# Performance work log

Hardware: AMD Instinct MI355X
Metric: run time of the kernel (lower is better)

Reference implementation:

```python
import jax, jax.numpy as jnp
import numpy as np

EMBED = 1024
HEADS = 16
HEAD_DIM = EMBED // HEADS
FFN_DIM = 4096
SEQ = 2048
BATCH = 2
EPS = 1e-5


def setup_inputs() -> dict:
    key = jax.random.key(0)
    ks = jax.random.split(key, 13)
    s = lambda n: 1.0 / np.sqrt(n)
    return {
        "x": jax.random.normal(ks[0], (BATCH, SEQ, EMBED), jnp.float32),
        # qkv projection (stored as [in, out])
        "w_qkv": jax.random.normal(ks[1], (EMBED, 3 * EMBED), jnp.float32) * s(EMBED),
        "b_qkv": jax.random.normal(ks[2], (3 * EMBED,), jnp.float32) * 0.02,
        "w_out": jax.random.normal(ks[3], (EMBED, EMBED), jnp.float32) * s(EMBED),
        "b_out": jax.random.normal(ks[4], (EMBED,), jnp.float32) * 0.02,
        # FFN
        "w_up": jax.random.normal(ks[5], (EMBED, FFN_DIM), jnp.float32) * s(EMBED),
        "b_up": jax.random.normal(ks[6], (FFN_DIM,), jnp.float32) * 0.02,
        "w_down": jax.random.normal(ks[7], (FFN_DIM, EMBED), jnp.float32) * s(FFN_DIM),
        "b_down": jax.random.normal(ks[8], (EMBED,), jnp.float32) * 0.02,
        # LayerNorms
        "g1": jnp.ones((EMBED,), jnp.float32),
        "be1": jnp.zeros((EMBED,), jnp.float32),
        "g2": jnp.ones((EMBED,), jnp.float32),
        "be2": jnp.zeros((EMBED,), jnp.float32),
    }


def _layernorm(x, g, b):
    mu = jnp.mean(x, axis=-1, keepdims=True)
    var = jnp.mean(jnp.square(x - mu), axis=-1, keepdims=True)
    return (x - mu) * jax.lax.rsqrt(var + EPS) * g + b


def reference(x, w_qkv, b_qkv, w_out, b_out, w_up, b_up, w_down, b_down, g1, be1, g2, be2):
    B, S, E = x.shape
    qkv = (x @ w_qkv + b_qkv).reshape(B, S, 3, HEADS, HEAD_DIM)
    qkv = jnp.transpose(qkv, (2, 0, 3, 1, 4))
    q, k, v = qkv[0], qkv[1], qkv[2]
    scale = 1.0 / jnp.sqrt(jnp.float32(HEAD_DIM))
    attn = jnp.einsum("bhqd,bhkd->bhqk", q, k) * scale  # [B,H,S,S]
    causal = jnp.tril(jnp.ones((S, S), bool))
    attn = jnp.where(causal, attn, -jnp.inf)
    attn = jax.nn.softmax(attn, axis=-1)
    out = jnp.einsum("bhqk,bhkd->bhqd", attn, v)  # [B,H,S,D]
    out = jnp.transpose(out, (0, 2, 1, 3)).reshape(B, S, E)
    attn_out = out @ w_out + b_out
    x = _layernorm(x + attn_out, g1, be1)
    ffn_out = jax.nn.relu(x @ w_up + b_up) @ w_down + b_down
    return _layernorm(x + ffn_out, g2, be2)
```

## Files before the change

### kernel.cpp

```cpp
#include <hip/hip_runtime.h>
#include <hip/hip_bf16.h>

#define EMBED 1024
#define HEADS 16
#define HDIM 64
#define FFN 4096
#define SEQ 2048
#define BATCH 2
#define MTOT (BATCH*SEQ)
#define QSCALE 0.1803368801111137f

typedef __attribute__((ext_vector_type(8))) short bf16x8;
typedef __attribute__((ext_vector_type(4))) float f32x4;
typedef __attribute__((ext_vector_type(16))) float f32x16;
typedef unsigned short u16;
typedef unsigned int u32;

__device__ __forceinline__ u16 f2bf(float f) {
  union { float f; unsigned u; } v; v.f = f;
  unsigned r = v.u + 0x7FFFu + ((v.u >> 16) & 1u);
  return (u16)(r >> 16);
}

__device__ __forceinline__ void async_ld16(const void* g, void* l) {
  __builtin_amdgcn_global_load_lds((const __attribute__((address_space(1))) void*)g,
                                   (__attribute__((address_space(3))) void*)l,
                                   16, 0, 0);
}

__global__ __launch_bounds__(256) void k_cvt(const float* __restrict__ in,
                                             u16* __restrict__ out, int n4) {
  int i = blockIdx.x * 256 + threadIdx.x;
  int st = gridDim.x * 256;
  for (; i < n4; i += st) {
    float4 v = ((const float4*)in)[i];
    ushort4 o;
    o.x = f2bf(v.x); o.y = f2bf(v.y); o.z = f2bf(v.z); o.w = f2bf(v.w);
    ((ushort4*)out)[i] = o;
  }
}

__global__ __launch_bounds__(256) void k_tr(const float* __restrict__ w,
                                            u16* __restrict__ wT, int K, int N) {
  __shared__ u16 tile[32][33];
  int n0 = blockIdx.x * 32, k0 = blockIdx.y * 32;
  int tx = threadIdx.x, ty = threadIdx.y;
  #pragma unroll
  for (int i = 0; i < 4; ++i) {
    int k = k0 + ty + i * 8;
    tile[ty + i * 8][tx] = f2bf(w[(size_t)k * N + n0 + tx]);
  }
  __syncthreads();
  #pragma unroll
  for (int i = 0; i < 4; ++i) {
    int n = n0 + ty + i * 8;
    wT[(size_t)n * K + k0 + tx] = tile[tx][ty + i * 8];
  }
}

__global__ __launch_bounds__(256) void k_vtr(const u16* __restrict__ V,
                                             u16* __restrict__ Vt) {
  __shared__ u16 t[64][72];
  const int s0 = blockIdx.x * 64;
  const size_t ib = (size_t)blockIdx.y * (size_t)SEQ * HDIM;
  const size_t ob = (size_t)blockIdx.y * (size_t)HDIM * SEQ;
  const int tid = threadIdx.x;
  const int r = tid >> 2, c0 = (tid & 3) * 16;
  bf16x8 v0 = *(const bf16x8*)(V + ib + (size_t)(s0 + r) * HDIM + c0);
  bf16x8 v1 = *(const bf16x8*)(V + ib + (size_t)(s0 + r) * HDIM + c0 + 8);
  #pragma unroll
  for (int j = 0; j < 8; ++j) {
    t[c0 + j][r] = (u16)v0[j];
    t[c0 + 8 + j][r] = (u16)v1[j];
  }
  __syncthreads();
  const int d = tid >> 2, sc = (tid & 3) * 16;
  bf16x8 o0, o1;
  #pragma unroll
  for (int j = 0; j < 8; ++j) { o0[j] = t[d][sc + j]; o1[j] = t[d][sc + 8 + j]; }
  *(bf16x8*)(Vt + ob + (size_t)d * SEQ + s0 + sc) = o0;
  *(bf16x8*)(Vt + ob + (size_t)d * SEQ + s0 + sc + 8) = o1;
}

template <int BN, int BK, int OMODE, bool RELU>
__global__ __launch_bounds__(256) void k_gemm(
    const u16* __restrict__ A, const u16* __restrict__ BT,
    const float* __restrict__ bias,
    void* __restrict__ out0, void* __restrict__ out1, void* __restrict__ out2,
    int M, int N, int K) {
  constexpr int NR = BN / 32;
  constexpr int KS = BK / 32;
  constexpr int TPR = BK / 8;
  constexpr int RPI = 256 / TPR;
  constexpr int CM = TPR - 1;

  __shared__ u16 As[2][128 * BK];
  __shared__ u16 Bs[2][BN * BK];
  const int tid = threadIdx.x;
  const int lane = tid & 63, g = lane >> 4, li = lane & 15;
  const int wid = tid >> 6, wm = wid >> 1, wn = wid & 1;

  const int gx = gridDim.x;
  const int nwg = gx * gridDim.y;
  const int flat = blockIdx.y * gx + blockIdx.x;
  const int cpx = nwg >> 3;
  const int swz = (flat & 7) * cpx + (flat >> 3);
  const int m0 = (swz / gx) * 128, n0 = (swz % gx) * BN;

  f32x4 acc[4][NR] = {};

  const u16* Ablk = A + (size_t)m0 * K;
  const u16* Bblk = BT + (size_t)n0 * K;
  const int srow = tid / TPR;
  const int scol = ((tid % TPR) ^ (srow & CM)) * 8;

  auto stage = [&](int buf, int kt) {
    #pragma unroll
    for (int r = 0; r < 128; r += RPI)
      async_ld16(Ablk + (size_t)(srow + r) * K + kt + scol, &As[buf][(srow + r) * BK] + (tid % TPR) * 8);
    #pragma unroll
    for (int r = 0; r < BN; r += RPI)
      async_ld16(Bblk + (size_t)(srow + r) * K + kt + scol, &Bs[buf][(srow + r) * BK] + (tid % TPR) * 8);
  };

  stage(0, 0);
  int cur = 0;
  for (int kt = 0; kt < K; kt += BK) {
    __syncthreads();
    if (kt + BK < K) stage(cur ^ 1, kt + BK);

    bf16x8 af[4][KS], bfr[NR][KS];
    #pragma unroll
    for (int i = 0; i < 4; ++i) {
      const int row = wm * 64 + i * 16 + li;
      #pragma unroll
      for (int ks = 0; ks < KS; ++ks) {
        const int c = ks * 4 + g;
        af[i][ks] = *(const bf16x8*)(&As[cur][row * BK] + ((c ^ (row & CM)) & CM) * 8);
      }
    }
    #pragma unroll
    for (int j = 0; j < NR; ++j) {
      const int row = wn * (BN / 2) + j * 16 + li;
      #pragma unroll
      for (int ks = 0; ks < KS; ++ks) {
        const int c = ks * 4 + g;
        bfr[j][ks] = *(const bf16x8*)(&Bs[cur][row * BK] + ((c ^ (row & CM)) & CM) * 8);
      }
    }
    #pragma unroll
    for (int ks = 0; ks < KS; ++ks)
      #pragma unroll
      for (int i = 0; i < 4; ++i)
        #pragma unroll
        for (int j = 0; j < NR; ++j)
          acc[i][j] = __builtin_amdgcn_mfma_f32_16x16x32_bf16(af[i][ks], bfr[j][ks], acc[i][j], 0, 0, 0);
    cur ^= 1;
  }

  float bcol[NR];
  #pragma unroll
  for (int j = 0; j < NR; ++j) bcol[j] = bias[n0 + wn * (BN / 2) + j * 16 + li];

  #pragma unroll
  for (int i = 0; i < 4; ++i) {
    #pragma unroll
    for (int j = 0; j < NR; ++j) {
      #pragma unroll
      for (int r = 0; r < 4; ++r) {
        int row = m0 + wm * 64 + i * 16 + g * 4 + r;
        int col = n0 + wn * (BN / 2) + j * 16 + li;
        float v = acc[i][j][r] + bcol[j];
        if (RELU) v = fmaxf(v, 0.f);
        if (OMODE == 0) {
          ((u16*)out0)[(size_t)row * N + col] = f2bf(v);
        } else if (OMODE == 1) {
          ((float*)out0)[(size_t)row * N + col] = v;
        } else {
          int which = col >> 10, hh = (col >> 6) & 15, d = col & 63;
          int bb = row >> 11, ss = row & 2047;
          if (which == 0) v *= QSCALE;
          u16* dst = which == 0 ? (u16*)out0 : (which == 1 ? (u16*)out1 : (u16*)out2);
          dst[((size_t)((bb * 16 + hh) * 2048 + ss)) * 64 + d] = f2bf(v);
        }
      }
    }
  }
}

__global__ __launch_bounds__(256, 3) void k_attn6(
    const u16* __restrict__ Q, const u16* __restrict__ K,
    const u16* __restrict__ Vt, u16* __restrict__ ctx) {
  const int bh = blockIdx.x;
  const int t32 = 63 - (int)blockIdx.y;
  const int b = bh >> 4, h = bh & 15;
  const int tid = threadIdx.x;
  const int wid = tid >> 6, lane = tid & 63;
  const int ql = lane & 31, hl = lane >> 5;

  __shared__ __align__(16) float mrg[3][64][34];

  const int wq0 = t32 * 32;
  const int qg = wq0 + ql;
  const int nt = ((wq0 + 31) >> 6) + 1;

  const size_t kbase = (size_t)bh * SEQ * HDIM;
  const size_t vbase = (size_t)bh * HDIM * SEQ;

  bf16x8 qf[4];
  #pragma unroll
  for (int d4 = 0; d4 < 4; ++d4)
    qf[d4] = *(const bf16x8*)(Q + kbase + (size_t)qg * HDIM + d4 * 16 + hl * 8);

  const u16* kp = K + kbase + (size_t)ql * HDIM + hl * 8;
  const u16* vp = Vt + vbase + (size_t)ql * SEQ + hl * 8;

  f32x16 o0 = {}, o1 = {};
  float m_run = -1e30f, l_run = 0.f;

  for (int kt = wid; kt < nt; kt += 4) {
    const bool kh1 = (kt * 64 + 32 <= wq0 + 31);
    const bool domask = (kt * 64 + (kh1 ? 63 : 31) > wq0);
    const int koff = kt * 64 * HDIM;

    bf16x8 kf0[4], kf1[4];
    #pragma unroll
    for (int d4 = 0; d4 < 4; ++d4) {
      kf0[d4] = *(const bf16x8*)(kp + koff + d4 * 16);
      if (kh1) kf1[d4] = *(const bf16x8*)(kp + koff + 32 * HDIM + d4 * 16);
    }
    bf16x8 vf0[4], vf1[4];
    #pragma unroll
    for (int t = 0; t < 4; ++t)
      if (t < 2 || kh1) {
        vf0[t] = *(const bf16x8*)(vp + kt * 64 + t * 16);
        vf1[t] = *(const bf16x8*)(vp + 32 * SEQ + kt * 64 + t * 16);
      }

    f32x16 S0 = {}, S1 = {};
    #pragma unroll
    for (int d4 = 0; d4 < 4; ++d4)
      S0 = __builtin_amdgcn_mfma_f32_32x32x16_bf16(kf0[d4], qf[d4], S0, 0, 0, 0);
    if (kh1) {
      #pragma unroll
      for (int d4 = 0; d4 < 4; ++d4)
        S1 = __builtin_amdgcn_mfma_f32_32x32x16_bf16(kf1[d4], qf[d4], S1, 0, 0, 0);
    }

    if (domask) {
      const int qrel = qg - kt * 64 - 4 * hl;
      #pragma unroll
      for (int r = 0; r < 16; ++r) {
        const int kc = (r & 3) + 8 * (r >> 2);
        S0[r] = (kc <= qrel) ? S0[r] : -3.0e38f;
      }
      if (kh1) {
        #pragma unroll
        for (int r = 0; r < 16; ++r) {
          const int kc = 32 + (r & 3) + 8 * (r >> 2);
          S1[r] = (kc <= qrel) ? S1[r] : -3.0e38f;
        }
      }
    }

    float mt = -3.0e38f;
    #pragma unroll
    for (int r = 0; r < 16; ++r) mt = fmaxf(mt, S0[r]);
    if (kh1) {
      #pragma unroll
      for (int r = 0; r < 16; ++r) mt = fmaxf(mt, S1[r]);
    }
    mt = fmaxf(mt, __shfl_xor(mt, 32, 64));

    if (!__all(mt <= m_run + 8.0f)) {
      const float mn = fmaxf(m_run, mt);
      const float alpha = exp2f(m_run - mn);
      l_run *= alpha;
      o0 *= alpha;
      o1 *= alpha;
      m_run = mn;
    }
    float sum = 0.f;
    #pragma unroll
    for (int r = 0; r < 16; ++r) { S0[r] = exp2f(S0[r] - m_run); sum += S0[r]; }
    if (kh1) {
      #pragma unroll
      for (int r = 0; r < 16; ++r) { S1[r] = exp2f(S1[r] - m_run); sum += S1[r]; }
    }
    sum += __shfl_xor(sum, 32, 64);
    l_run += sum;

    u32 pk[2][8], sw[2][8];
    #pragma unroll
    for (int m = 0; m < 4; ++m) {
      asm("v_cvt_pk_bf16_f32 %0, %1, %2" : "=v"(pk[0][2*m])   : "v"(S0[4*m+0]), "v"(S0[4*m+1]));
      asm("v_cvt_pk_bf16_f32 %0, %1, %2" : "=v"(pk[0][2*m+1]) : "v"(S0[4*m+2]), "v"(S0[4*m+3]));
    }
    #pragma unroll
    for (int i = 0; i < 8; ++i) sw[0][i] = __shfl_xor(pk[0][i], 32, 64);
    if (kh1) {
      #pragma unroll
      for (int m = 0; m < 4; ++m) {
        asm("v_cvt_pk_bf16_f32 %0, %1, %2" : "=v"(pk[1][2*m])   : "v"(S1[4*m+0]), "v"(S1[4*m+1]));
        asm("v_cvt_pk_bf16_f32 %0, %1, %2" : "=v"(pk[1][2*m+1]) : "v"(S1[4*m+2]), "v"(S1[4*m+3]));
      }
      #pragma unroll
      for (int i = 0; i < 8; ++i) sw[1][i] = __shfl_xor(pk[1][i], 32, 64);
    }

    #pragma unroll
    for (int t = 0; t < 4; ++t) {
      if (t < 2 || kh1) {
        const int c = t >> 1, m0 = 2 * (t & 1), m1 = m0 + 1;
        union { u32 u[4]; bf16x8 v; } pf;
        pf.u[0] = hl ? sw[c][2*m1]   : pk[c][2*m0];
        pf.u[1] = hl ? sw[c][2*m1+1] : pk[c][2*m0+1];
        pf.u[2] = hl ? pk[c][2*m1]   : sw[c][2*m0];
        pf.u[3] = hl ? pk[c][2*m1+1] : sw[c][2*m0+1];
        o0 = __builtin_amdgcn_mfma_f32_32x32x16_bf16(vf0[t], pf.v, o0, 0, 0, 0);
        o1 = __builtin_amdgcn_mfma_f32_32x32x16_bf16(vf1[t], pf.v, o1, 0, 0, 0);
      }
    }
  }

  if (wid > 0) {
    float* p = &mrg[wid - 1][lane][0];
    *(f32x16*)(p) = o0;
    *(f32x16*)(p + 16) = o1;
    p[32] = m_run;
    p[33] = l_run;
  }
  __syncthreads();
  if (wid > 0) return;

  float M = m_run;
  #pragma unroll
  for (int w = 0; w < 3; ++w) M = fmaxf(M, mrg[w][lane][32]);
  const float fa = exp2f(m_run - M);
  f32x16 acc0 = o0 * fa, acc1 = o1 * fa;
  float L = l_run * fa;
  #pragma unroll
  for (int w = 0; w < 3; ++w) {
    const float* p = &mrg[w][lane][0];
    const float fw = exp2f(p[32] - M);
    L += p[33] * fw;
    f32x16 t0 = *(const f32x16*)(p);
    f32x16 t1 = *(const f32x16*)(p + 16);
    acc0 += t0 * fw;
    acc1 += t1 * fw;
  }
  const float inv = 1.f / L;

  u16* outp = ctx + (size_t)(b * SEQ + qg) * EMBED + h * HDIM + 4 * hl;
  #pragma unroll
  for (int m = 0; m < 4; ++m) {
    ushort4 s0v, s1v;
    s0v.x = f2bf(acc0[4*m+0] * inv); s0v.y = f2bf(acc0[4*m+1] * inv);
    s0v.z = f2bf(acc0[4*m+2] * inv); s0v.w = f2bf(acc0[4*m+3] * inv);
    *(ushort4*)(outp + 8 * m) = s0v;
    s1v.x = f2bf(acc1[4*m+0] * inv); s1v.y = f2bf(acc1[4*m+1] * inv);
    s1v.z = f2bf(acc1[4*m+2] * inv); s1v.w = f2bf(acc1[4*m+3] * inv);
    *(ushort4*)(outp + 32 + 8 * m) = s1v;
  }
}

__global__ __launch_bounds__(256) void k_add_ln(
    const float* __restrict__ a, const float* __restrict__ bmat,
    const float* __restrict__ gam, const float* __restrict__ bet,
    float* __restrict__ outf, u16* __restrict__ outb) {
  const int row = blockIdx.x;
  const int t = threadIdx.x;
  __shared__ float red[8];
  float4 va = ((const float4*)(a + (size_t)row * EMBED))[t];
  float4 vb = ((const float4*)(bmat + (size_t)row * EMBED))[t];
  float s0 = va.x + vb.x, s1 = va.y + vb.y, s2 = va.z + vb.z, s3 = va.w + vb.w;
  float sum = s0 + s1 + s2 + s3;
  float sq = s0 * s0 + s1 * s1 + s2 * s2 + s3 * s3;
  #pragma unroll
  for (int m = 1; m < 64; m <<= 1) {
    sum += __shfl_xor(sum, m, 64);
    sq += __shfl_xor(sq, m, 64);
  }
  int wid = t >> 6;
  if ((t & 63) == 0) { red[wid] = sum; red[4 + wid] = sq; }
  __syncthreads();
  sum = red[0] + red[1] + red[2] + red[3];
  sq = red[4] + red[5] + red[6] + red[7];
  float mean = sum * (1.f / EMBED);
  float var = sq * (1.f / EMBED) - mean * mean;
  float rstd = rsqrtf(var + 1e-5f);
  float4 gv = ((const float4*)gam)[t], bev = ((const float4*)bet)[t];
  float y0 = (s0 - mean) * rstd * gv.x + bev.x;
  float y1 = (s1 - mean) * rstd * gv.y + bev.y;
  float y2 = (s2 - mean) * rstd * gv.z + bev.z;
  float y3 = (s3 - mean) * rstd * gv.w + bev.w;
  float4 o; o.x = y0; o.y = y1; o.z = y2; o.w = y3;
  ((float4*)(outf + (size_t)row * EMBED))[t] = o;
  if (outb) {
    ushort4 ob; ob.x = f2bf(y0); ob.y = f2bf(y1); ob.z = f2bf(y2); ob.w = f2bf(y3);
    ((ushort4*)(outb + (size_t)row * EMBED))[t] = ob;
  }
}

extern "C" void kernel_launch(void* const* d_in, const int* in_sizes, int n_in,
                              void* d_out, int out_size, void* d_ws, size_t ws_size,
                              hipStream_t stream) {
  const float* x      = (const float*)d_in[0];
  const float* w_qkv  = (const float*)d_in[1];
  const float* b_qkv  = (const float*)d_in[2];
  const float* w_out  = (const float*)d_in[3];
  const float* b_out  = (const float*)d_in[4];
  const float* w_up   = (const float*)d_in[5];
  const float* b_up   = (const float*)d_in[6];
  const float* w_down = (const float*)d_in[7];
  const float* b_down = (const float*)d_in[8];
  const float* g1  = (const float*)d_in[9];
  const float* be1 = (const float*)d_in[10];
  const float* g2  = (const float*)d_in[11];
  const float* be2 = (const float*)d_in[12];

  char* ws = (char*)d_ws;
  size_t off = 0;
  auto alloc = [&](size_t bytes) { void* p = ws + off; off += (bytes + 255) & ~(size_t)255; return p; };

  u16* xb     = (u16*)alloc((size_t)MTOT * EMBED * 2);
  u16* wqkvT  = (u16*)alloc((size_t)3 * EMBED * EMBED * 2);
  u16* woutT  = (u16*)alloc((size_t)EMBED * EMBED * 2);
  u16* wupT   = (u16*)alloc((size_t)FFN * EMBED * 2);
  u16* wdownT = (u16*)alloc((size_t)EMBED * FFN * 2);
  u16* qb     = (u16*)alloc((size_t)MTOT * EMBED * 2);
  u16* kb     = (u16*)alloc((size_t)MTOT * EMBED * 2);
  u16* vb     = (u16*)alloc((size_t)MTOT * EMBED * 2);
  u16* vtb    = (u16*)alloc((size_t)MTOT * EMBED * 2);
  u16* ctx    = (u16*)alloc((size_t)MTOT * EMBED * 2);
  float* attn_proj = (float*)alloc((size_t)MTOT * EMBED * 4);
  float* y_f32     = (float*)alloc((size_t)MTOT * EMBED * 4);
  u16* y_bf16      = (u16*)alloc((size_t)MTOT * EMBED * 2);
  u16* hmid        = (u16*)alloc((size_t)MTOT * FFN * 2);
  float* ffn_o     = (float*)alloc((size_t)MTOT * EMBED * 4);

  dim3 trb(32, 8);
  k_cvt<<<2048, 256, 0, stream>>>(x, xb, MTOT * EMBED / 4);
  k_tr<<<dim3(3 * EMBED / 32, EMBED / 32), trb, 0, stream>>>(w_qkv, wqkvT, EMBED, 3 * EMBED);
  k_tr<<<dim3(EMBED / 32, EMBED / 32), trb, 0, stream>>>(w_out, woutT, EMBED, EMBED);
  k_tr<<<dim3(FFN / 32, EMBED / 32), trb, 0, stream>>>(w_up, wupT, EMBED, FFN);
  k_tr<<<dim3(EMBED / 32, FFN / 32), trb, 0, stream>>>(w_down, wdownT, FFN, EMBED);

  k_gemm<128, 32, 2, false><<<dim3(3 * EMBED / 128, MTOT / 128), 256, 0, stream>>>(
      xb, wqkvT, b_qkv, qb, kb, vb, MTOT, 3 * EMBED, EMBED);

  k_vtr<<<dim3(SEQ / 64, BATCH * HEADS), 256, 0, stream>>>(vb, vtb);

  k_attn6<<<dim3(BATCH * HEADS, 64), 256, 0, stream>>>(qb, kb, vtb, ctx);

  k_gemm<64, 64, 1, false><<<dim3(EMBED / 64, MTOT / 128), 256, 0, stream>>>(
      ctx, woutT, b_out, attn_proj, nullptr, nullptr, MTOT, EMBED, EMBED);

  k_add_ln<<<MTOT, 256, 0, stream>>>(x, attn_proj, g1, be1, y_f32, y_bf16);

  k_gemm<128, 32, 0, true><<<dim3(FFN / 128, MTOT / 128), 256, 0, stream>>>(
      y_bf16, wupT, b_up, hmid, nullptr, nullptr, MTOT, FFN, EMBED);

  k_gemm<64, 64, 1, false><<<dim3(EMBED / 64, MTOT / 128), 256, 0, stream>>>(
      hmid, wdownT, b_down, ffn_o, nullptr, nullptr, MTOT, EMBED, FFN);

  k_add_ln<<<MTOT, 256, 0, stream>>>(y_f32, ffn_o, g2, be2, (float*)d_out, nullptr);

  (void)in_sizes; (void)n_in; (void)out_size; (void)ws_size;
}
```

Baseline: 277.8 us.

## Add 256x256-tile 8-wave GEMM with ping-pong staging for QKV and FFN-up

```diff
diff --git a/kernel.cpp b/kernel.cpp
--- a/kernel.cpp
+++ b/kernel.cpp
@@ -80,6 +80,141 @@
   for (int j = 0; j < 8; ++j) { o0[j] = t[d][sc + j]; o1[j] = t[d][sc + 8 + j]; }
   *(bf16x8*)(Vt + ob + (size_t)d * SEQ + s0 + sc) = o0;
   *(bf16x8*)(Vt + ob + (size_t)d * SEQ + s0 + sc + 8) = o1;
+}
+
+template <int OMODE, bool RELU>
+__global__ __launch_bounds__(512) void k_gemm8(
+    const u16* __restrict__ A, const u16* __restrict__ BT,
+    const float* __restrict__ bias,
+    void* __restrict__ out0, void* __restrict__ out1, void* __restrict__ out2,
+    int M, int N, int K) {
+  __shared__ __align__(16) u16 As[2][2][128 * 64];
+  __shared__ __align__(16) u16 Bs[2][2][128 * 64];
+  const int tid = threadIdx.x;
+  const int lane = tid & 63, g = lane >> 4, li = lane & 15;
+  const int wid = tid >> 6, wm = wid >> 2, wn = wid & 3;
+
+  const int gx = gridDim.x;
+  const int nwg = gx * gridDim.y;
+  const int flat = blockIdx.y * gx + blockIdx.x;
+  const int cpx = nwg >> 3;
+  const int swz = (flat & 7) * cpx + (flat >> 3);
+  const int m0 = (swz / gx) * 256, n0 = (swz % gx) * 256;
+
+  f32x4 acc[8][4] = {};
+
+  const u16* Ablk = A + (size_t)m0 * K;
+  const u16* Bblk = BT + (size_t)n0 * K;
+  const int trow = tid >> 3;
+  const int sc = (tid & 7) ^ (trow & 7);
+
+  auto stageA = [&](int buf, int h, int kt) {
+    #pragma unroll
+    for (int r = 0; r < 2; ++r)
+      async_ld16(Ablk + (size_t)(h * 64 + r * 128 + trow) * K + kt + sc * 8,
+                 &As[buf][h][0] + r * 4096 + tid * 8);
+  };
+  auto stageB = [&](int buf, int h, int kt) {
+    #pragma unroll
+    for (int r = 0; r < 2; ++r) {
+      const int p = trow + r * 64;
+      async_ld16(Bblk + (size_t)(((p >> 5) << 6) + h * 32 + (p & 31)) * K + kt + sc * 8,
+                 &Bs[buf][h][0] + r * 4096 + tid * 8);
+    }
+  };
+
+#define VM4_ asm volatile("s_waitcnt vmcnt(4)" ::: "memory")
+#define VM2_ asm volatile("s_waitcnt vmcnt(2)" ::: "memory")
+#define VM0_ asm volatile("s_waitcnt vmcnt(0)" ::: "memory")
+#define VMN_
+#define GP8(IH, JH, VMSTMT, STAGE_STMT) do {                                   \
+    bf16x8 a_[4][2], b_[2][2];                                                 \
+    _Pragma("unroll")                                                          \
+    for (int i2 = 0; i2 < 4; ++i2) {                                           \
+      const int pa = wm * 64 + i2 * 16 + li;                                   \
+      _Pragma("unroll")                                                        \
+      for (int ks = 0; ks < 2; ++ks)                                           \
+        a_[i2][ks] = *(const bf16x8*)(&As[cur][IH][0] + pa * 64 +              \
+                                      (((ks * 4 + g) ^ (li & 7)) * 8));        \
+    }                                                                          \
+    _Pragma("unroll")                                                          \
+    for (int j2 = 0; j2 < 2; ++j2) {                                           \
+      const int pb = wn * 32 + j2 * 16 + li;                                   \
+      _Pragma("unroll")                                                        \
+      for (int ks = 0; ks < 2; ++ks)                                           \
+        b_[j2][ks] = *(const bf16x8*)(&Bs[cur][JH][0] + pb * 64 +              \
+                                      (((ks * 4 + g) ^ (li & 7)) * 8));        \
+    }                                                                          \
+    STAGE_STMT;                                                                \
+    VMSTMT;                                                                    \
+    __builtin_amdgcn_s_barrier();                                              \
+    asm volatile("s_waitcnt lgkmcnt(0)" ::: "memory");                         \
+    __builtin_amdgcn_sched_barrier(0);                                         \
+    __builtin_amdgcn_s_setprio(1);                                             \
+    _Pragma("unroll")                                                          \
+    for (int ks = 0; ks < 2; ++ks)                                             \
+      _Pragma("unroll")                                                        \
+      for (int i2 = 0; i2 < 4; ++i2)                                           \
+        _Pragma("unroll")                                                      \
+        for (int j2 = 0; j2 < 2; ++j2)                                         \
+          acc[IH * 4 + i2][JH * 2 + j2] = __builtin_amdgcn_mfma_f32_16x16x32_bf16( \
+              a_[i2][ks], b_[j2][ks], acc[IH * 4 + i2][JH * 2 + j2], 0, 0, 0); \
+    __builtin_amdgcn_s_setprio(0);                                             \
+    __builtin_amdgcn_s_barrier();                                              \
+    asm volatile("" ::: "memory");                                             \
+  } while (0)
+
+  stageA(0, 0, 0); stageB(0, 0, 0); stageA(0, 1, 0); stageB(0, 1, 0);
+  VM4_;
+  __builtin_amdgcn_s_barrier();
+  asm volatile("" ::: "memory");
+
+  int cur = 0;
+  const int nkt = K >> 6;
+  for (int t = 0; t < nkt - 1; ++t) {
+    const int kn = (t + 1) * 64;
+    GP8(0, 0, VM4_, stageA(cur ^ 1, 0, kn));
+    GP8(1, 0, VM4_, stageB(cur ^ 1, 0, kn));
+    GP8(0, 1, VMN_, stageA(cur ^ 1, 1, kn));
+    GP8(1, 1, VM4_, stageB(cur ^ 1, 1, kn));
+    cur ^= 1;
+  }
+  GP8(0, 0, VM2_, );
+  GP8(1, 0, VM0_, );
+  GP8(0, 1, VMN_, );
+  GP8(1, 1, VMN_, );
+#undef GP8
+#undef VM4_
+#undef VM2_
+#undef VM0_
+#undef VMN_
+
+  float bcol[4];
+  #pragma unroll
+  for (int j = 0; j < 4; ++j) bcol[j] = bias[n0 + wn * 64 + j * 16 + li];
+
+  #pragma unroll
+  for (int i = 0; i < 8; ++i) {
+    #pragma unroll
+    for (int j = 0; j < 4; ++j) {
+      #pragma unroll
+      for (int r = 0; r < 4; ++r) {
+        int row = m0 + wm * 128 + i * 16 + g * 4 + r;
+        int col = n0 + wn * 64 + j * 16 + li;
+        float v = acc[i][j][r] + bcol[j];
+        if (RELU) v = fmaxf(v, 0.f);
+        if (OMODE == 0) {
+          ((u16*)out0)[(size_t)row * N + col] = f2bf(v);
+        } else {
+          int which = col >> 10, hh = (col >> 6) & 15, d = col & 63;
+          int bb = row >> 11, ss = row & 2047;
+          if (which == 0) v *= QSCALE;
+          u16* dst = which == 0 ? (u16*)out0 : (which == 1 ? (u16*)out1 : (u16*)out2);
+          dst[((size_t)((bb * 16 + hh) * 2048 + ss)) * 64 + d] = f2bf(v);
+        }
+      }
+    }
+  }
 }
 
 template <int BN, int BK, int OMODE, bool RELU>
@@ -446,7 +581,7 @@
   k_tr<<<dim3(FFN / 32, EMBED / 32), trb, 0, stream>>>(w_up, wupT, EMBED, FFN);
   k_tr<<<dim3(EMBED / 32, FFN / 32), trb, 0, stream>>>(w_down, wdownT, FFN, EMBED);
 
-  k_gemm<128, 32, 2, false><<<dim3(3 * EMBED / 128, MTOT / 128), 256, 0, stream>>>(
+  k_gemm8<2, false><<<dim3(3 * EMBED / 256, MTOT / 256), 512, 0, stream>>>(
       xb, wqkvT, b_qkv, qb, kb, vb, MTOT, 3 * EMBED, EMBED);
 
   k_vtr<<<dim3(SEQ / 64, BATCH * HEADS), 256, 0, stream>>>(vb, vtb);
@@ -458,7 +593,7 @@
 
   k_add_ln<<<MTOT, 256, 0, stream>>>(x, attn_proj, g1, be1, y_f32, y_bf16);
 
-  k_gemm<128, 32, 0, true><<<dim3(FFN / 128, MTOT / 128), 256, 0, stream>>>(
+  k_gemm8<0, true><<<dim3(FFN / 256, MTOT / 256), 512, 0, stream>>>(
       y_bf16, wupT, b_up, hmid, nullptr, nullptr, MTOT, FFN, EMBED);
 
   k_gemm<64, 64, 1, false><<<dim3(EMBED / 64, MTOT / 128), 256, 0, stream>>>(
```

After: 266.9 us. 3.9% less time.
